# Kernel tuning notes

Measured on AMD Instinct MI355X. Metric: run time of the kernel, lower is better.

Reference implementation:

```python
import jax, jax.numpy as jnp
import numpy as np
import math

B, S, DIM = 1, 2048, 2048
H, KVH, HD = 32, 8, 64
REP = H // KVH


def _rope_cache(seqlen, head_dim, base=10000.0):
    # (seqlen, 2*head_dim): [cos | sin], each duplicated across both halves
    inv_freq = 1.0 / (base ** (np.arange(0, head_dim, 2, dtype=np.float32) / head_dim))
    t = np.arange(seqlen, dtype=np.float32)
    ang = np.outer(t, inv_freq)                    # (S, HD/2)
    ang = np.concatenate([ang, ang], axis=-1)      # (S, HD)
    return jnp.asarray(np.concatenate([np.cos(ang), np.sin(ang)], axis=-1))


def setup_inputs() -> dict:
    key = jax.random.key(0)
    ks = jax.random.split(key, 12)
    std = 0.02
    return {
        "x": jax.random.normal(ks[0], (B, S, DIM), jnp.float32),
        "rope_cache": _rope_cache(S, HD),
        "wq_w": jax.random.normal(ks[1], (H * HD, DIM), jnp.float32) * std,
        "wq_b": jax.random.normal(ks[2], (H * HD,), jnp.float32) * std,
        "wk_w": jax.random.normal(ks[3], (KVH * HD, DIM), jnp.float32) * std,
        "wk_b": jax.random.normal(ks[4], (KVH * HD,), jnp.float32) * std,
        "wv_w": jax.random.normal(ks[5], (KVH * HD, DIM), jnp.float32) * std,
        "wv_b": jax.random.normal(ks[6], (KVH * HD,), jnp.float32) * std,
        "wo_w": jax.random.normal(ks[7], (DIM, H * HD), jnp.float32) * std,
        "wo_b": jax.random.normal(ks[8], (DIM,), jnp.float32) * std,
        "sinks": jax.random.normal(ks[9], (H,), jnp.float32) * std,
    }


def _rotate_half(t):
    h = t.shape[-1] // 2
    return jnp.concatenate([-t[..., h:], t[..., :h]], axis=-1)


def reference(x, rope_cache, wq_w, wq_b, wk_w, wk_b, wv_w, wv_b, wo_w, wo_b, sinks):
    bsz, seqlen, _ = x.shape
    q = (jnp.einsum('bsd,od->bso', x, wq_w) + wq_b).reshape(bsz, seqlen, H, HD)
    k = (jnp.einsum('bsd,od->bso', x, wk_w) + wk_b).reshape(bsz, seqlen, KVH, HD)
    v = (jnp.einsum('bsd,od->bso', x, wv_w) + wv_b).reshape(bsz, seqlen, KVH, HD)

    cos = rope_cache[:seqlen, :HD][None, :, None, :]
    sin = rope_cache[:seqlen, HD:][None, :, None, :]
    q = q * cos + _rotate_half(q) * sin
    k = k * cos + _rotate_half(k) * sin

    # repeat_kv: repeat_interleave along head dim
    k = jnp.repeat(k, REP, axis=2)  # (B,S,H,HD)
    v = jnp.repeat(v, REP, axis=2)

    q = q.transpose(0, 2, 1, 3)  # (B,H,S,HD)
    k = k.transpose(0, 2, 1, 3)
    v = v.transpose(0, 2, 1, 3)

    scale = 1.0 / math.sqrt(HD)
    scores = jnp.einsum('bhqd,bhkd->bhqk', q, k) * scale
    causal = jnp.tril(jnp.ones((seqlen, seqlen), dtype=bool))
    scores = jnp.where(causal, scores, -jnp.inf)

    m = jnp.max(scores, axis=-1, keepdims=True)
    lse = m[..., 0] + jnp.log(jnp.sum(jnp.exp(scores - m), axis=-1))  # (B,H,S)
    attn = jnp.exp(scores - lse[..., None])
    out = jnp.einsum('bhqk,bhkd->bhqd', attn, v)

    # sink-token LSE renormalization
    combined_lse = jnp.logaddexp(lse, sinks[None, :, None])
    renorm = jnp.exp(jnp.clip(lse - combined_lse, -20.0, 0.0))
    out = out * renorm[..., None]

    out = out.transpose(0, 2, 1, 3).reshape(bsz, seqlen, H * HD)
    return jnp.einsum('bso,do->bsd', out, wo_w) + wo_b
```

## Files before the change

### kernel.cpp

```cpp
#include <hip/hip_runtime.h>


#define S_LEN 2048
#define DIM_  2048
#define QK_LD 2560

typedef __attribute__((ext_vector_type(8))) __bf16 bf16x8;
typedef __attribute__((ext_vector_type(4))) float f32x4;
typedef __attribute__((ext_vector_type(4))) unsigned short us4;

__device__ __forceinline__ unsigned short f2bf(float f) {
    union { float f; unsigned u; } v; v.f = f;
    unsigned r = v.u + 0x7FFFu + ((v.u >> 16) & 1u);
    return (unsigned short)(r >> 16);
}
__device__ __forceinline__ float bf2f(unsigned short u) {
    union { unsigned u; float f; } v; v.u = ((unsigned)u) << 16;
    return v.f;
}

__device__ __forceinline__ void gload_lds16(const void* g, void* l) {
    __builtin_amdgcn_global_load_lds(
        (const __attribute__((address_space(1))) void*)g,
        (__attribute__((address_space(3))) void*)l, 16, 0, 0);
}

__device__ __forceinline__ int swz32(int r, int ch) { return r*32 + ((ch ^ ((r >> 1) & 3)) << 3); }
__device__ __forceinline__ int swz64(int r, int ch) { return r*64 + ((ch ^ (r & 7)) << 3); }

__global__ void cvt_all(const float* __restrict__ x,  const float* __restrict__ wq,
                        const float* __restrict__ wk, const float* __restrict__ wv,
                        const float* __restrict__ wo,
                        unsigned short* __restrict__ xb,
                        unsigned short* __restrict__ wqkv,
                        unsigned short* __restrict__ wob) {
    const int i4 = blockIdx.x * 256 + threadIdx.x;
    const float* src; unsigned short* dst; int off;
    if (i4 < 1048576)      { src = x;  dst = xb;             off = i4; }
    else if (i4 < 2097152) { src = wq; dst = wqkv;           off = i4 - 1048576; }
    else if (i4 < 2359296) { src = wk; dst = wqkv + 4194304; off = i4 - 2097152; }
    else if (i4 < 2621440) { src = wv; dst = wqkv + 5242880; off = i4 - 2359296; }
    else                   { src = wo; dst = wob;            off = i4 - 2621440; }
    const float4 v = reinterpret_cast<const float4*>(src)[off];
    us4 o = { f2bf(v.x), f2bf(v.y), f2bf(v.z), f2bf(v.w) };
    reinterpret_cast<us4*>(dst)[off] = o;
}

__global__ void build_bias(const float* __restrict__ qb, const float* __restrict__ kb,
                           const float* __restrict__ vb, float* __restrict__ out) {
    const int i = blockIdx.x * 256 + threadIdx.x;
    if (i < 2048) out[i] = qb[i];
    else if (i < 2560) out[i] = kb[i - 2048];
    else if (i < 3072) out[i] = vb[i - 2560];
}

template<int MODE>
__global__ __launch_bounds__(256)
void gemm_bt(const unsigned short* __restrict__ A,
             const unsigned short* __restrict__ B,
             const float* __restrict__ bias,
             unsigned short* __restrict__ Cqk,
             unsigned short* __restrict__ Vt,
             float* __restrict__ Cf,
             int K)
{
    __shared__ unsigned short As[2][128 * 32];
    __shared__ unsigned short Bs[2][128 * 32];
    const int t = threadIdx.x;
    const int lane = t & 63;
    const int w = t >> 6;
    const int wr = w >> 1, wc = w & 1;
    const int lq = lane & 15;
    const int g = lane >> 4;
    const int m0 = blockIdx.y * 128;
    const int n0 = blockIdx.x * 128;

    const f32x4 z = {0.f, 0.f, 0.f, 0.f};
    f32x4 acc[4][4];
    #pragma unroll
    for (int i = 0; i < 4; i++)
        #pragma unroll
        for (int j = 0; j < 4; j++) acc[i][j] = z;

    auto stage = [&](int buf, int k0) {
        #pragma unroll
        for (int c = 0; c < 2; c++) {
            const int chunk = w * 128 + c * 64 + lane;
            const int r = chunk >> 2;
            const int chl = (chunk & 3) ^ ((r >> 1) & 3);
            gload_lds16(&A[(size_t)(m0 + r) * K + k0 + (chl << 3)],
                        &As[buf][(size_t)(w * 128 + c * 64) * 8]);
            gload_lds16(&B[(size_t)(n0 + r) * K + k0 + (chl << 3)],
                        &Bs[buf][(size_t)(w * 128 + c * 64) * 8]);
        }
    };

    stage(0, 0);
    __syncthreads();
    const int NIT = K >> 5;
    for (int it = 0; it < NIT; ++it) {
        const int cur = it & 1;
        if (it + 1 < NIT) stage(cur ^ 1, (it + 1) << 5);
        bf16x8 a[4], b[4];
        #pragma unroll
        for (int mi = 0; mi < 4; mi++)
            a[mi] = *reinterpret_cast<const bf16x8*>(&As[cur][swz32(wr * 64 + mi * 16 + lq, g)]);
        #pragma unroll
        for (int ni = 0; ni < 4; ni++)
            b[ni] = *reinterpret_cast<const bf16x8*>(&Bs[cur][swz32(wc * 64 + ni * 16 + lq, g)]);
        #pragma unroll
        for (int mi = 0; mi < 4; mi++)
            #pragma unroll
            for (int ni = 0; ni < 4; ni++)
                acc[mi][ni] = __builtin_amdgcn_mfma_f32_16x16x32_bf16(a[mi], b[ni], acc[mi][ni], 0, 0, 0);
        __syncthreads();
    }

    #pragma unroll
    for (int mi = 0; mi < 4; mi++) {
        const int row0 = m0 + wr * 64 + mi * 16 + g * 4;
        #pragma unroll
        for (int ni = 0; ni < 4; ni++) {
            const int col = n0 + wc * 64 + ni * 16 + lq;
            const float bv = bias[col];
            if (MODE == 1) {
                #pragma unroll
                for (int j = 0; j < 4; j++)
                    Cf[(size_t)(row0 + j) * 2048 + col] = acc[mi][ni][j] + bv;
            } else {
                if (col < 2560) {
                    const float qs = (col < 2048) ? 0.1803368801f : 1.0f;
                    #pragma unroll
                    for (int j = 0; j < 4; j++)
                        Cqk[(size_t)(row0 + j) * QK_LD + col] = f2bf((acc[mi][ni][j] + bv) * qs);
                } else {
                    us4 pk;
                    #pragma unroll
                    for (int j = 0; j < 4; j++) pk[j] = f2bf(acc[mi][ni][j] + bv);
                    *reinterpret_cast<us4*>(&Vt[(size_t)(col - 2560) * S_LEN + row0]) = pk;
                }
            }
        }
    }
}

__global__ void rope_kernel(unsigned short* __restrict__ qk, const float* __restrict__ rope) {
    const int idx = blockIdx.x * 256 + threadIdx.x;
    const int s = idx / 1280;
    const int rem = idx - s * 1280;
    const int head = rem >> 5;
    const int p = rem & 31;
    const size_t base = (size_t)s * QK_LD + head * 64 + p;
    const float c = rope[s * 128 + p];
    const float sn = rope[s * 128 + 64 + p];
    const float x0 = bf2f(qk[base]);
    const float x1 = bf2f(qk[base + 32]);
    qk[base]      = f2bf(x0 * c - x1 * sn);
    qk[base + 32] = f2bf(x1 * c + x0 * sn);
}

__global__ __launch_bounds__(256)
void attn_kernel(const unsigned short* __restrict__ qk,
                 const unsigned short* __restrict__ vt,
                 const float* __restrict__ sinks,
                 unsigned short* __restrict__ aout)
{
    const int qb  = 31 - blockIdx.x;
    const int h   = blockIdx.y;
    const int hkv = h >> 2;
    const int t = threadIdx.x;
    const int lane = t & 63;
    const int w = t >> 6;
    const int lq = lane & 15;
    const int g = lane >> 4;

    __shared__ unsigned short Ks[2][64 * 64];
    __shared__ unsigned short Vs[2][64 * 64];
    __shared__ unsigned short Ps[4][16 * 64];
    unsigned short* Pw = &Ps[w][0];

    const int qrow = qb * 64 + w * 16 + lq;

    bf16x8 aq[2];
    #pragma unroll
    for (int c = 0; c < 2; c++)
        aq[c] = *reinterpret_cast<const bf16x8*>(&qk[(size_t)qrow * QK_LD + h * 64 + c * 32 + g * 8]);

    const f32x4 z = {0.f, 0.f, 0.f, 0.f};
    f32x4 acc[4];
    #pragma unroll
    for (int df = 0; df < 4; df++) acc[df] = z;
    float m = -1e30f, l = 0.f;

    bf16x8 kreg[2], vreg[2];
    #pragma unroll
    for (int i = 0; i < 2; i++) {
        const int e = i * 256 + t, r = e >> 3, ch = e & 7;
        kreg[i] = *reinterpret_cast<const bf16x8*>(&qk[(size_t)r * QK_LD + 2048 + hkv * 64 + (ch << 3)]);
        vreg[i] = *reinterpret_cast<const bf16x8*>(&vt[(size_t)(hkv * 64 + r) * S_LEN + (ch << 3)]);
    }
    #pragma unroll
    for (int i = 0; i < 2; i++) {
        const int e = i * 256 + t, r = e >> 3, ch = e & 7;
        *reinterpret_cast<bf16x8*>(&Ks[0][swz64(r, ch)]) = kreg[i];
        *reinterpret_cast<bf16x8*>(&Vs[0][swz64(r, ch)]) = vreg[i];
    }
    __syncthreads();

    for (int tkv = 0; tkv <= qb; tkv++) {
        const int cur = tkv & 1;
        if (tkv < qb) {
            const int kvn = (tkv + 1) * 64;
            #pragma unroll
            for (int i = 0; i < 2; i++) {
                const int e = i * 256 + t, r = e >> 3, ch = e & 7;
                kreg[i] = *reinterpret_cast<const bf16x8*>(&qk[(size_t)(kvn + r) * QK_LD + 2048 + hkv * 64 + (ch << 3)]);
                vreg[i] = *reinterpret_cast<const bf16x8*>(&vt[(size_t)(hkv * 64 + r) * S_LEN + kvn + (ch << 3)]);
            }
        }

        f32x4 sc[4];
        #pragma unroll
        for (int f = 0; f < 4; f++) {
            sc[f] = z;
            #pragma unroll
            for (int c = 0; c < 2; c++) {
                const bf16x8 bk = *reinterpret_cast<const bf16x8*>(&Ks[cur][swz64(f * 16 + lq, c * 4 + g)]);
                sc[f] = __builtin_amdgcn_mfma_f32_16x16x32_bf16(bk, aq[c], sc[f], 0, 0, 0);
            }
        }

        if (tkv == qb) {
            const int thr = w * 16 + lq - g * 4;
            #pragma unroll
            for (int f = 0; f < 4; f++)
                #pragma unroll
                for (int j = 0; j < 4; j++)
                    if (f * 16 + j > thr) sc[f][j] = -1e30f;
        }

        float mx = sc[0][0];
        #pragma unroll
        for (int f = 0; f < 4; f++)
            #pragma unroll
            for (int j = 0; j < 4; j++) mx = fmaxf(mx, sc[f][j]);
        mx = fmaxf(mx, __shfl_xor(mx, 16));
        mx = fmaxf(mx, __shfl_xor(mx, 32));
        const float mn = fmaxf(m, mx);
        const float rs = exp2f(m - mn);
        m = mn;
        float s = 0.f;
        #pragma unroll
        for (int f = 0; f < 4; f++)
            #pragma unroll
            for (int j = 0; j < 4; j++) {
                const float p = exp2f(sc[f][j] - mn);
                sc[f][j] = p;
                s += p;
            }
        s += __shfl_xor(s, 16);
        s += __shfl_xor(s, 32);
        l = l * rs + s;
        #pragma unroll
        for (int df = 0; df < 4; df++) acc[df] *= rs;

        #pragma unroll
        for (int f = 0; f < 4; f++) {
            us4 pk = { f2bf(sc[f][0]), f2bf(sc[f][1]), f2bf(sc[f][2]), f2bf(sc[f][3]) };
            *reinterpret_cast<us4*>(
                &Pw[lq * 64 + ((((f << 1) | (g >> 1)) ^ (lq & 7)) << 3) + ((g & 1) << 2)]) = pk;
        }
        #pragma unroll
        for (int c = 0; c < 2; c++) {
            const bf16x8 pb = *reinterpret_cast<const bf16x8*>(
                &Pw[lq * 64 + (((c * 4 + g) ^ (lq & 7)) << 3)]);
            #pragma unroll
            for (int df = 0; df < 4; df++) {
                const bf16x8 bv = *reinterpret_cast<const bf16x8*>(&Vs[cur][swz64(df * 16 + lq, c * 4 + g)]);
                acc[df] = __builtin_amdgcn_mfma_f32_16x16x32_bf16(bv, pb, acc[df], 0, 0, 0);
            }
        }

        if (tkv < qb) {
            #pragma unroll
            for (int i = 0; i < 2; i++) {
                const int e = i * 256 + t, r = e >> 3, ch = e & 7;
                *reinterpret_cast<bf16x8*>(&Ks[cur ^ 1][swz64(r, ch)]) = kreg[i];
                *reinterpret_cast<bf16x8*>(&Vs[cur ^ 1][swz64(r, ch)]) = vreg[i];
            }
        }
        __syncthreads();
    }

    const float sink = sinks[h];
    const float lse = 0.6931471806f * (m + log2f(l));
    const float d = sink - lse;
    float f = (d > 20.f) ? d : log1pf(__expf(d));
    if (f > 20.f) f = 20.f;
    const float fac = __expf(-f) / l;
    #pragma unroll
    for (int df = 0; df < 4; df++) {
        us4 pk = { f2bf(acc[df][0] * fac), f2bf(acc[df][1] * fac),
                   f2bf(acc[df][2] * fac), f2bf(acc[df][3] * fac) };
        *reinterpret_cast<us4*>(&aout[(size_t)qrow * DIM_ + h * 64 + df * 16 + g * 4]) = pk;
    }
}

extern "C" void kernel_launch(void* const* d_in, const int* in_sizes, int n_in,
                              void* d_out, int out_size, void* d_ws, size_t ws_size,
                              hipStream_t stream) {
    const float* x     = (const float*)d_in[0];
    const float* rope  = (const float*)d_in[1];
    const float* wq_w  = (const float*)d_in[2];
    const float* wq_b  = (const float*)d_in[3];
    const float* wk_w  = (const float*)d_in[4];
    const float* wk_b  = (const float*)d_in[5];
    const float* wv_w  = (const float*)d_in[6];
    const float* wv_b  = (const float*)d_in[7];
    const float* wo_w  = (const float*)d_in[8];
    const float* wo_b  = (const float*)d_in[9];
    const float* sinks = (const float*)d_in[10];
    float* out = (float*)d_out;

    char* ws = (char*)d_ws;
    unsigned short* xb    = (unsigned short*)(ws);
    unsigned short* wqkv  = (unsigned short*)(ws + (8u  << 20));
    unsigned short* wob   = (unsigned short*)(ws + (20u << 20));
    unsigned short* qkbuf = (unsigned short*)(ws + (28u << 20));
    unsigned short* vtbuf = (unsigned short*)(ws + (38u << 20));
    unsigned short* abuf  = (unsigned short*)(ws + (40u << 20));
    float*          bcat  = (float*)(ws + (48u << 20));

    cvt_all<<<14336, 256, 0, stream>>>(x, wq_w, wk_w, wv_w, wo_w, xb, wqkv, wob);
    build_bias<<<12, 256, 0, stream>>>(wq_b, wk_b, wv_b, bcat);

    gemm_bt<0><<<dim3(24, 16), 256, 0, stream>>>(xb, wqkv, bcat, qkbuf, vtbuf, nullptr, 2048);
    rope_kernel<<<10240, 256, 0, stream>>>(qkbuf, rope);
    attn_kernel<<<dim3(32, 32), 256, 0, stream>>>(qkbuf, vtbuf, sinks, abuf);
    gemm_bt<1><<<dim3(16, 16), 256, 0, stream>>>(abuf, wob, wo_b, nullptr, nullptr, out, 2048);
}
```

Measured before the change: 288.0 us.

## Split attention KV across two blocks, add combine kernel, triple-buffer GEMM

The attention kernel now splits each query tile's KV range between two blocks that take alternating 64-row tiles. Each block writes an unnormalized partial accumulator plus its running max and sum, and a new combine kernel merges the two halves and applies the sink renormalization. The goal is more blocks and better balance across causal tiles. K/V tiles are now loaded straight into LDS with global_load_lds, replacing register staging. The GEMM moves from double to triple buffering, using explicit vmcnt waits and a single barrier per iteration. The costs are an extra kernel launch, a round trip of partial results through bf16 that adds rounding error, and more LDS use in the GEMM.

```diff
diff --git a/kernel.cpp b/kernel.cpp
--- a/kernel.cpp
+++ b/kernel.cpp
@@ -64,8 +64,8 @@
              float* __restrict__ Cf,
              int K)
 {
-    __shared__ unsigned short As[2][128 * 32];
-    __shared__ unsigned short Bs[2][128 * 32];
+    __shared__ unsigned short As[3][128 * 32];
+    __shared__ unsigned short Bs[3][128 * 32];
     const int t = threadIdx.x;
     const int lane = t & 63;
     const int w = t >> 6;
@@ -95,12 +95,15 @@
         }
     };
 
+    const int NIT = K >> 5;
     stage(0, 0);
-    __syncthreads();
-    const int NIT = K >> 5;
+    stage(1, 32);
     for (int it = 0; it < NIT; ++it) {
-        const int cur = it & 1;
-        if (it + 1 < NIT) stage(cur ^ 1, (it + 1) << 5);
+        if (it + 1 < NIT) asm volatile("s_waitcnt vmcnt(4)" ::: "memory");
+        else              asm volatile("s_waitcnt vmcnt(0)" ::: "memory");
+        __builtin_amdgcn_s_barrier();
+        if (it + 2 < NIT) stage((it + 2) % 3, (it + 2) << 5);
+        const int cur = it % 3;
         bf16x8 a[4], b[4];
         #pragma unroll
         for (int mi = 0; mi < 4; mi++)
@@ -113,7 +116,6 @@
             #pragma unroll
             for (int ni = 0; ni < 4; ni++)
                 acc[mi][ni] = __builtin_amdgcn_mfma_f32_16x16x32_bf16(a[mi], b[ni], acc[mi][ni], 0, 0, 0);
-        __syncthreads();
     }
 
     #pragma unroll
@@ -162,11 +164,13 @@
 __global__ __launch_bounds__(256)
 void attn_kernel(const unsigned short* __restrict__ qk,
                  const unsigned short* __restrict__ vt,
-                 const float* __restrict__ sinks,
-                 unsigned short* __restrict__ aout)
+                 unsigned short* __restrict__ pacc,
+                 float* __restrict__ pml)
 {
-    const int qb  = 31 - blockIdx.x;
-    const int h   = blockIdx.y;
+    const int bx = blockIdx.x;
+    const int c = bx & 1;
+    const int qb = 31 - (bx >> 1);
+    const int h = blockIdx.y;
     const int hkv = h >> 2;
     const int t = threadIdx.x;
     const int lane = t & 63;
@@ -183,8 +187,14 @@
 
     bf16x8 aq[2];
     #pragma unroll
-    for (int c = 0; c < 2; c++)
-        aq[c] = *reinterpret_cast<const bf16x8*>(&qk[(size_t)qrow * QK_LD + h * 64 + c * 32 + g * 8]);
+    for (int cc = 0; cc < 2; cc++)
+        aq[cc] = *reinterpret_cast<const bf16x8*>(&qk[(size_t)qrow * QK_LD + h * 64 + cc * 32 + g * 8]);
+    {
+        const uint4 u0 = reinterpret_cast<const uint4&>(aq[0]);
+        const uint4 u1 = reinterpret_cast<const uint4&>(aq[1]);
+        asm volatile("" :: "v"(u0.x), "v"(u0.y), "v"(u0.z), "v"(u0.w),
+                           "v"(u1.x), "v"(u1.y), "v"(u1.z), "v"(u1.w));
+    }
 
     const f32x4 z = {0.f, 0.f, 0.f, 0.f};
     f32x4 acc[4];
@@ -192,45 +202,41 @@
     for (int df = 0; df < 4; df++) acc[df] = z;
     float m = -1e30f, l = 0.f;
 
-    bf16x8 kreg[2], vreg[2];
-    #pragma unroll
-    for (int i = 0; i < 2; i++) {
-        const int e = i * 256 + t, r = e >> 3, ch = e & 7;
-        kreg[i] = *reinterpret_cast<const bf16x8*>(&qk[(size_t)r * QK_LD + 2048 + hkv * 64 + (ch << 3)]);
-        vreg[i] = *reinterpret_cast<const bf16x8*>(&vt[(size_t)(hkv * 64 + r) * S_LEN + (ch << 3)]);
-    }
-    #pragma unroll
-    for (int i = 0; i < 2; i++) {
-        const int e = i * 256 + t, r = e >> 3, ch = e & 7;
-        *reinterpret_cast<bf16x8*>(&Ks[0][swz64(r, ch)]) = kreg[i];
-        *reinterpret_cast<bf16x8*>(&Vs[0][swz64(r, ch)]) = vreg[i];
-    }
-    __syncthreads();
-
-    for (int tkv = 0; tkv <= qb; tkv++) {
-        const int cur = tkv & 1;
-        if (tkv < qb) {
-            const int kvn = (tkv + 1) * 64;
-            #pragma unroll
-            for (int i = 0; i < 2; i++) {
-                const int e = i * 256 + t, r = e >> 3, ch = e & 7;
-                kreg[i] = *reinterpret_cast<const bf16x8*>(&qk[(size_t)(kvn + r) * QK_LD + 2048 + hkv * 64 + (ch << 3)]);
-                vreg[i] = *reinterpret_cast<const bf16x8*>(&vt[(size_t)(hkv * 64 + r) * S_LEN + kvn + (ch << 3)]);
-            }
-        }
+    auto stage = [&](int buf, int tv) {
+        const int kv0 = tv * 64;
+        #pragma unroll
+        for (int i = 0; i < 2; i++) {
+            const int chunk = i * 256 + w * 64 + lane;
+            const int r = chunk >> 3;
+            const int chl = (chunk & 7) ^ (r & 7);
+            gload_lds16(&qk[(size_t)(kv0 + r) * QK_LD + 2048 + hkv * 64 + (chl << 3)],
+                        &Ks[buf][(size_t)(i * 256 + w * 64) * 8]);
+            gload_lds16(&vt[(size_t)(hkv * 64 + r) * S_LEN + kv0 + (chl << 3)],
+                        &Vs[buf][(size_t)(i * 256 + w * 64) * 8]);
+        }
+    };
+
+    const int ntile = (qb >= c) ? ((qb - c) >> 1) + 1 : 0;
+    if (ntile > 0) stage(0, c);
+    int cur = 0;
+    for (int i = 0; i < ntile; ++i) {
+        const int tv = c + 2 * i;
+        asm volatile("s_waitcnt vmcnt(0)" ::: "memory");
+        __builtin_amdgcn_s_barrier();
+        if (i + 1 < ntile) stage(cur ^ 1, tv + 2);
 
         f32x4 sc[4];
         #pragma unroll
         for (int f = 0; f < 4; f++) {
             sc[f] = z;
             #pragma unroll
-            for (int c = 0; c < 2; c++) {
-                const bf16x8 bk = *reinterpret_cast<const bf16x8*>(&Ks[cur][swz64(f * 16 + lq, c * 4 + g)]);
-                sc[f] = __builtin_amdgcn_mfma_f32_16x16x32_bf16(bk, aq[c], sc[f], 0, 0, 0);
+            for (int cc = 0; cc < 2; cc++) {
+                const bf16x8 bk = *reinterpret_cast<const bf16x8*>(&Ks[cur][swz64(f * 16 + lq, cc * 4 + g)]);
+                sc[f] = __builtin_amdgcn_mfma_f32_16x16x32_bf16(bk, aq[cc], sc[f], 0, 0, 0);
             }
         }
 
-        if (tkv == qb) {
+        if (tv == qb) {
             const int thr = w * 16 + lq - g * 4;
             #pragma unroll
             for (int f = 0; f < 4; f++)
@@ -271,38 +277,62 @@
                 &Pw[lq * 64 + ((((f << 1) | (g >> 1)) ^ (lq & 7)) << 3) + ((g & 1) << 2)]) = pk;
         }
         #pragma unroll
-        for (int c = 0; c < 2; c++) {
+        for (int cc = 0; cc < 2; cc++) {
             const bf16x8 pb = *reinterpret_cast<const bf16x8*>(
-                &Pw[lq * 64 + (((c * 4 + g) ^ (lq & 7)) << 3)]);
+                &Pw[lq * 64 + (((cc * 4 + g) ^ (lq & 7)) << 3)]);
             #pragma unroll
             for (int df = 0; df < 4; df++) {
-                const bf16x8 bv = *reinterpret_cast<const bf16x8*>(&Vs[cur][swz64(df * 16 + lq, c * 4 + g)]);
+                const bf16x8 bv = *reinterpret_cast<const bf16x8*>(&Vs[cur][swz64(df * 16 + lq, cc * 4 + g)]);
                 acc[df] = __builtin_amdgcn_mfma_f32_16x16x32_bf16(bv, pb, acc[df], 0, 0, 0);
             }
         }
-
-        if (tkv < qb) {
-            #pragma unroll
-            for (int i = 0; i < 2; i++) {
-                const int e = i * 256 + t, r = e >> 3, ch = e & 7;
-                *reinterpret_cast<bf16x8*>(&Ks[cur ^ 1][swz64(r, ch)]) = kreg[i];
-                *reinterpret_cast<bf16x8*>(&Vs[cur ^ 1][swz64(r, ch)]) = vreg[i];
-            }
-        }
-        __syncthreads();
-    }
-
-    const float sink = sinks[h];
-    const float lse = 0.6931471806f * (m + log2f(l));
-    const float d = sink - lse;
+        cur ^= 1;
+    }
+
+    const size_t rbase = ((size_t)(h * 2 + c) * 2048 + qrow);
+    #pragma unroll
+    for (int df = 0; df < 4; df++) {
+        us4 pk = { f2bf(acc[df][0]), f2bf(acc[df][1]), f2bf(acc[df][2]), f2bf(acc[df][3]) };
+        *reinterpret_cast<us4*>(&pacc[rbase * 64 + df * 16 + g * 4]) = pk;
+    }
+    if (g == 0) {
+        pml[rbase * 2]     = m;
+        pml[rbase * 2 + 1] = l;
+    }
+}
+
+__global__ void attn_combine(const unsigned short* __restrict__ pacc,
+                             const float* __restrict__ pml,
+                             const float* __restrict__ sinks,
+                             unsigned short* __restrict__ abuf) {
+    const int idx = blockIdx.x * 256 + threadIdx.x;
+    const int q4 = idx & 3;
+    const int row = (idx >> 2) & 2047;
+    const int h = idx >> 13;
+    const size_t r0 = (size_t)(h * 2 + 0) * 2048 + row;
+    const size_t r1 = (size_t)(h * 2 + 1) * 2048 + row;
+    const float m0 = pml[r0 * 2], l0 = pml[r0 * 2 + 1];
+    const float m1 = pml[r1 * 2], l1 = pml[r1 * 2 + 1];
+    const float M = fmaxf(m0, m1);
+    const float w0 = exp2f(m0 - M), w1 = exp2f(m1 - M);
+    const float L = l0 * w0 + l1 * w1;
+    const float lse = 0.6931471806f * (M + log2f(L));
+    const float d = sinks[h] - lse;
     float f = (d > 20.f) ? d : log1pf(__expf(d));
     if (f > 20.f) f = 20.f;
-    const float fac = __expf(-f) / l;
-    #pragma unroll
-    for (int df = 0; df < 4; df++) {
-        us4 pk = { f2bf(acc[df][0] * fac), f2bf(acc[df][1] * fac),
-                   f2bf(acc[df][2] * fac), f2bf(acc[df][3] * fac) };
-        *reinterpret_cast<us4*>(&aout[(size_t)qrow * DIM_ + h * 64 + df * 16 + g * 4]) = pk;
+    const float fac = __expf(-f) / L;
+    const unsigned short* a0 = &pacc[r0 * 64 + q4 * 16];
+    const unsigned short* a1 = &pacc[r1 * 64 + q4 * 16];
+    unsigned short* dst = &abuf[(size_t)row * DIM_ + h * 64 + q4 * 16];
+    #pragma unroll
+    for (int k = 0; k < 4; k++) {
+        const us4 x0 = *reinterpret_cast<const us4*>(&a0[k * 4]);
+        const us4 x1 = *reinterpret_cast<const us4*>(&a1[k * 4]);
+        us4 r;
+        #pragma unroll
+        for (int j = 0; j < 4; j++)
+            r[j] = f2bf((bf2f(x0[j]) * w0 + bf2f(x1[j]) * w1) * fac);
+        *reinterpret_cast<us4*>(&dst[k * 4]) = r;
     }
 }
 
@@ -330,12 +360,15 @@
     unsigned short* vtbuf = (unsigned short*)(ws + (38u << 20));
     unsigned short* abuf  = (unsigned short*)(ws + (40u << 20));
     float*          bcat  = (float*)(ws + (48u << 20));
+    unsigned short* pacc  = (unsigned short*)(ws);
+    float*          pml   = (float*)(ws + (16u << 20));
 
     cvt_all<<<14336, 256, 0, stream>>>(x, wq_w, wk_w, wv_w, wo_w, xb, wqkv, wob);
     build_bias<<<12, 256, 0, stream>>>(wq_b, wk_b, wv_b, bcat);
 
     gemm_bt<0><<<dim3(24, 16), 256, 0, stream>>>(xb, wqkv, bcat, qkbuf, vtbuf, nullptr, 2048);
     rope_kernel<<<10240, 256, 0, stream>>>(qkbuf, rope);
-    attn_kernel<<<dim3(32, 32), 256, 0, stream>>>(qkbuf, vtbuf, sinks, abuf);
+    attn_kernel<<<dim3(64, 32), 256, 0, stream>>>(qkbuf, vtbuf, pacc, pml);
+    attn_combine<<<1024, 256, 0, stream>>>(pacc, pml, sinks, abuf);
     gemm_bt<1><<<dim3(16, 16), 256, 0, stream>>>(abuf, wob, wo_b, nullptr, nullptr, out, 2048);
 }
```

New measurement: 288.0 us. About the same (-0.0%).
